# Optimization experiments

Measured on AMD Instinct MI355X. Metric: run time of the kernel, lower is better.

Reference implementation:

```python
import jax, jax.numpy as jnp
import numpy as np

B, T, D, H = 2, 2048, 768, 12
d = D // H
FRAG, K_SEL, G = 16, 6, 4
TOP_U, PROTO = 12, 32
ALPHA, GAMMA = 0.2, 0.2
W_MEAN, W_MAX, W_TOPK, W_STD = 1.0, 0.6, 0.4, 0.2
TOPK_FRAC = 0.2
TAU = 8.0
NEG = -1e9


def _norm(x, eps=1e-6):
    return x / jnp.maximum(jnp.linalg.norm(x, axis=-1, keepdims=True), eps)


def setup_inputs():
    key = jax.random.key(0)
    ks = jax.random.split(key, 5)
    s = 0.02
    return {
        'x': jax.random.normal(ks[0], (B, T, D), jnp.float32),
        'Wq': jax.random.normal(ks[1], (D, D), jnp.float32) * s,
        'bq': jnp.zeros((D,), jnp.float32),
        'Wk': jax.random.normal(ks[2], (D, D), jnp.float32) * s,
        'bk': jnp.zeros((D,), jnp.float32),
        'Wv': jax.random.normal(ks[3], (D, D), jnp.float32) * s,
        'bv': jnp.zeros((D,), jnp.float32),
        'Wo': jax.random.normal(ks[4], (D, D), jnp.float32) * s,
        'bo': jnp.zeros((D,), jnp.float32),
    }


def _forward(x, Wq, bq, Wk, bk, Wv, bv, Wo, bo):
    scaling = d ** -0.5

    def shape(t):  # [B,T,D] -> [B*H,T,d]  (BartAttention._shape layout: (b,h))
        return t.reshape(B, T, H, d).transpose(0, 2, 1, 3).reshape(B * H, T, d)

    q = shape((x @ Wq.T + bq) * scaling)
    k = shape(x @ Wk.T + bk)
    v = shape(x @ Wv.T + bv)

    # ---- windowed local candidate indices (build_indices_encoder) ----
    half = FRAG // 2
    t_ar = jnp.arange(T)
    starts = jnp.clip(t_ar - half, 0, T - FRAG)
    idx = starts[:, None] + jnp.arange(FRAG)[None, :]            # [T,F]
    prior = jnp.exp(-jnp.abs(idx - t_ar[:, None]).astype(jnp.float32) / TAU)

    keys_win = k[:, idx]                                          # [BH,T,F,d]
    scores_win = jnp.einsum('btd,btfd->btf', q, keys_win)
    blended = scores_win + ALPHA * prior[None]

    # ---- greedy diversity-penalized top-k (WindowSelector.select_greedy) ----
    kvn = _norm(keys_win)
    f_ar = jnp.arange(FRAG)
    tmp = blended
    sels = []
    for r in range(K_SEL):
        j = jnp.argmax(tmp, -1)                                   # [BH,T]
        sels.append(j)
        if r < K_SEL - 1:
            sel_vec = jnp.take_along_axis(kvn, j[:, :, None, None], axis=2)[:, :, 0]
            cos = jnp.maximum(jnp.sum(kvn * sel_vec[:, :, None, :], -1), 0.0)
            tmp = tmp - GAMMA * cos
        tmp = jnp.where(f_ar[None, None, :] == j[..., None], NEG, tmp)
    sel_local = jnp.stack(sels, -1)                               # [BH,T,k]
    sel_abs = jnp.take_along_axis(
        jnp.broadcast_to(idx[None], (B * H, T, FRAG)), sel_local, axis=-1)

    # ---- per-head global tokens (GlobalChooser.choose_packed) ----
    # faithful to torch: key_states.view(H, bsz, Tk, d).mean(dim=1)
    Kmean = k.reshape(H, B, T, d).mean(1)
    Kbar = _norm(Kmean)
    q_summary = _norm(q.reshape(H, B, T, d).mean(1))
    idxp = jnp.round(jnp.linspace(0.0, T - 1, PROTO)).astype(jnp.int32)
    Qp = q_summary[:, idxp]                                       # [H,P,d]
    S = jax.nn.relu(jnp.einsum('hkd,hpd->hkp', Kbar, Qp))         # [H,T,P]
    kq = max(1, int(round(PROTO * TOPK_FRAC)))
    u = (W_MEAN * S.mean(-1) + W_MAX * S.max(-1)
         + W_TOPK * jax.lax.top_k(S, kq)[0].mean(-1)
         + W_STD * jnp.std(S, axis=-1, ddof=1))
    U = min(TOP_U, T)
    u_vals, top_idx = jax.lax.top_k(u, U)                         # [H,U]
    S_sub = jnp.take_along_axis(S, top_idx[:, :, None], axis=1)   # [H,U,P]
    hr = jnp.arange(H)
    m = jnp.zeros((H, PROTO), S.dtype)
    blocked = jnp.zeros((H, U), bool)
    chosen = []
    for r in range(G):  # greedy facility-location
        gains = jnp.maximum(S_sub - m[:, None, :], 0.0).sum(-1)
        gains = jnp.where(blocked, NEG, gains)
        j = jnp.argmax(gains, 1)
        chosen.append(j)
        blocked = blocked.at[hr, j].set(True)
        m = jnp.maximum(m, S_sub[hr, j])
    chosen_abs = jnp.take_along_axis(top_idx, jnp.stack(chosen, 1), axis=1)  # [H,G]

    # ---- sparse attention over local + global candidates ----
    glob = jnp.broadcast_to(chosen_abs[None], (B, H, G)).reshape(B * H, G)
    cand = jnp.concatenate(
        [sel_abs, jnp.broadcast_to(glob[:, None, :], (B * H, T, G))], -1)  # [BH,T,k+g]
    Ksel = jax.vmap(lambda kk, ii: kk[ii])(k, cand)               # [BH,T,k+g,d]
    Vsel = jax.vmap(lambda vv, ii: vv[ii])(v, cand)
    attn = jax.nn.softmax(jnp.einsum('btd,btcd->btc', q, Ksel), axis=-1)
    out = jnp.einsum('btc,btcd->btd', attn, Vsel)
    out = out.reshape(B, H, T, d).transpose(0, 2, 1, 3).reshape(B, T, D)
    return out @ Wo.T + bo


def reference(x, Wq, bq, Wk, bk, Wv, bv, Wo, bo):
    return _forward(x, Wq, bq, Wk, bk, Wv, bv, Wo, bo)
```

## Files before the change

kernel.cpp:

```cpp
#include <hip/hip_runtime.h>
#include <math.h>

#define TSEQ 2048
#define DM   768
#define NH   12
#define HD   64
#define NBH  24
#define WN   589824

typedef __attribute__((ext_vector_type(8))) short short8;
typedef __attribute__((ext_vector_type(8))) _Float16 half8;
typedef __attribute__((ext_vector_type(4))) float f32x4;

#define MFMA_F16(a, b, c)  __builtin_amdgcn_mfma_f32_16x16x32_f16(a, b, c, 0, 0, 0)

__constant__ int c_idxp[32] = {0,66,132,198,264,330,396,462,528,594,660,726,
  792,858,924,990,1057,1123,1189,1255,1321,1387,1453,1519,1585,1651,1717,1783,
  1849,1915,1981,2047};

template <int CTRL>
__device__ __forceinline__ float dppf(float x) {
  return __int_as_float(__builtin_amdgcn_mov_dpp(__float_as_int(x), CTRL, 0xF, 0xF, true));
}
template <int CTRL>
__device__ __forceinline__ int dppi(int x) {
  return __builtin_amdgcn_mov_dpp(x, CTRL, 0xF, 0xF, true);
}
__device__ __forceinline__ float wsum(float v) {
  v += dppf<0x121>(v);
  v += dppf<0x122>(v);
  v += dppf<0x124>(v);
  v += dppf<0x128>(v);
  v += __shfl_xor(v, 16, 64);
  v += __shfl_xor(v, 32, 64);
  return v;
}
__device__ __forceinline__ float rowsum16(float v) {
  v += dppf<0x121>(v); v += dppf<0x122>(v);
  v += dppf<0x124>(v); v += dppf<0x128>(v);
  return v;
}
__device__ __forceinline__ float rowmax16(float v) {
  v = fmaxf(v, dppf<0x121>(v)); v = fmaxf(v, dppf<0x122>(v));
  v = fmaxf(v, dppf<0x124>(v)); v = fmaxf(v, dppf<0x128>(v));
  return v;
}
__device__ __forceinline__ int rowmin16i(int v) {
  v = min(v, dppi<0x121>(v)); v = min(v, dppi<0x122>(v));
  v = min(v, dppi<0x124>(v)); v = min(v, dppi<0x128>(v));
  return v;
}

__device__ __forceinline__ void split16(const float4& v0, const float4& v1,
                                        ushort* ph, ushort* pl) {
  float xs[8] = {v0.x, v0.y, v0.z, v0.w, v1.x, v1.y, v1.z, v1.w};
  half8 h, l;
#pragma unroll
  for (int j = 0; j < 8; ++j) {
    _Float16 hb = (_Float16)xs[j];
    h[j] = hb;
    float d = xs[j] - (float)hb;
    l[j] = (_Float16)d;
  }
  *(half8*)ph = h;
  *(half8*)pl = l;
}

__device__ __forceinline__ int lds_idx(int row, int chunk ) {
  int line = row >> 1;
  int c8 = ((row & 1) << 2) | chunk;
  return line * 64 + ((c8 ^ (line & 7)) << 3);
}
__device__ __forceinline__ int qoff(int p, int c8) {
  return p * 64 + (((c8 ^ (p & 7)) & 7) << 3);
}

__global__ __launch_bounds__(256) void convert_kernel(
    const float* __restrict__ x,
    const float* __restrict__ W0, const float* __restrict__ W1,
    const float* __restrict__ W2, const float* __restrict__ W3,
    ushort* __restrict__ Xh, ushort* __restrict__ Xl,
    ushort* __restrict__ wsp) {
  int bid = blockIdx.x;
  if (bid < 1536) {
    size_t base = ((size_t)bid * 256 + threadIdx.x) * 8;
    float4 v0 = *(const float4*)(x + base);
    float4 v1 = *(const float4*)(x + base + 4);
    split16(v0, v1, Xh + base, Xl + base);
  } else {
    int r = bid - 1536;
    int mi = r / 288, sub = r - mi * 288;
    size_t base = ((size_t)sub * 256 + threadIdx.x) * 8;
    const float* s = (mi == 0) ? W0 : (mi == 1) ? W1 : (mi == 2) ? W2 : W3;
    ushort* h = wsp + (size_t)mi * 2 * WN;
    float4 v0 = *(const float4*)(s + base);
    float4 v1 = *(const float4*)(s + base + 4);
    split16(v0, v1, h + base, h + WN + base);
  }
}

template <int MODE, int NPROD>
__device__ __forceinline__ void gemm_mfma_body(
    const ushort* __restrict__ Agh, const ushort* __restrict__ Agl,
    const ushort* __restrict__ Bgh, const ushort* __restrict__ Bgl,
    const float* __restrict__ bias, float* __restrict__ dst, float scale,
    int mblk, int nblk, ushort* lds) {
  const int tid = threadIdx.x;
  const int lane = tid & 63;
  const int w = tid >> 6;
  const int wr = w >> 1, wc = w & 1;
  const int lrow = lane & 15, kq = lane >> 4;
  constexpr int ABUF = 4096;
  constexpr int BBUF = 2048;
  ushort* Ahs = lds;
  ushort* Als = Ahs + ABUF;
  ushort* Bhs = lds + 2 * ABUF;
  ushort* Bls = Bhs + BBUF;

  const int arow = tid >> 2;
  const int achk = tid & 3;
  const int aoff0 = lds_idx(arow, achk);
  const int aoff1 = lds_idx(arow + 64, achk);
  const int boff = lds_idx(arow, achk);

  const size_t a0 = (size_t)(mblk + arow) * DM + achk * 8;
  const size_t a1 = (size_t)(mblk + 64 + arow) * DM + achk * 8;
  const size_t b0 = (size_t)(nblk + arow) * DM + achk * 8;

  f32x4 acc[4][2];
#pragma unroll
  for (int i = 0; i < 4; ++i)
#pragma unroll
    for (int j = 0; j < 2; ++j) {
      f32x4 z = {0.f, 0.f, 0.f, 0.f};
      acc[i][j] = z;
    }

  short8 pah0 = *(const short8*)(Agh + a0), pah1 = *(const short8*)(Agh + a1);
  short8 pal0 = *(const short8*)(Agl + a0), pal1 = *(const short8*)(Agl + a1);
  short8 pbh = *(const short8*)(Bgh + b0);
  short8 pbl = *(const short8*)(Bgl + b0);

  for (int k0 = 0; k0 < DM; k0 += 32) {
    __syncthreads();
    *(short8*)&Ahs[aoff0] = pah0; *(short8*)&Ahs[aoff1] = pah1;
    *(short8*)&Als[aoff0] = pal0; *(short8*)&Als[aoff1] = pal1;
    *(short8*)&Bhs[boff] = pbh;
    *(short8*)&Bls[boff] = pbl;
    __syncthreads();
    if (k0 + 32 < DM) {
      pah0 = *(const short8*)(Agh + a0 + k0 + 32);
      pah1 = *(const short8*)(Agh + a1 + k0 + 32);
      pal0 = *(const short8*)(Agl + a0 + k0 + 32);
      pal1 = *(const short8*)(Agl + a1 + k0 + 32);
      pbh = *(const short8*)(Bgh + b0 + k0 + 32);
      pbl = *(const short8*)(Bgl + b0 + k0 + 32);
    }
    half8 afh[4], afl[4];
#pragma unroll
    for (int fi = 0; fi < 4; ++fi) {
      int o = lds_idx(wr * 64 + fi * 16 + lrow, kq);
      afh[fi] = *(const half8*)&Ahs[o];
      afl[fi] = *(const half8*)&Als[o];
    }
#pragma unroll
    for (int fj = 0; fj < 2; ++fj) {
      int o = lds_idx(wc * 32 + fj * 16 + lrow, kq);
      half8 bfh = *(const half8*)&Bhs[o];
      half8 bfl = *(const half8*)&Bls[o];
#pragma unroll
      for (int fi = 0; fi < 4; ++fi) {
        acc[fi][fj] = MFMA_F16(afh[fi], bfh, acc[fi][fj]);
        acc[fi][fj] = MFMA_F16(afl[fi], bfh, acc[fi][fj]);
        acc[fi][fj] = MFMA_F16(afh[fi], bfl, acc[fi][fj]);
        if (NPROD == 4) {
          acc[fi][fj] = MFMA_F16(afl[fi], bfl, acc[fi][fj]);
        }
      }
    }
  }

#pragma unroll
  for (int fj = 0; fj < 2; ++fj) {
    int col = nblk + wc * 32 + fj * 16 + lrow;
    float bv = bias[col];
#pragma unroll
    for (int fi = 0; fi < 4; ++fi) {
#pragma unroll
      for (int reg = 0; reg < 4; ++reg) {
        int row = mblk + wr * 64 + fi * 16 + kq * 4 + reg;
        float o = (acc[fi][fj][reg] + bv) * scale;
        if (MODE == 0) {
          dst[(size_t)row * DM + col] = o;
        } else {
          int b_ = row >> 11, t = row & (TSEQ - 1);
          int h = col >> 6, dd = col & 63;
          dst[(((size_t)(b_ * NH + h)) * TSEQ + t) * HD + dd] = o;
        }
      }
    }
  }
}

__global__ __launch_bounds__(256) void qkv_kernel(
    const ushort* __restrict__ Xh, const ushort* __restrict__ Xl,
    const ushort* __restrict__ wsp,
    const float* __restrict__ bq, float* __restrict__ qd,
    const float* __restrict__ bk, float* __restrict__ kd,
    const float* __restrict__ bv, float* __restrict__ vd) {
  __shared__ ushort lds[2 * 4096 + 2 * 2048];
  int lid = blockIdx.x + 12 * blockIdx.y + 384 * blockIdx.z;
  int swz = (lid & 7) * 144 + (lid >> 3);
  int z = swz / 384;
  int rem = swz - z * 384;
  int wy = rem / 12, wx = rem - wy * 12;
  const ushort* Bb = wsp + (size_t)z * 2 * WN;
  if (z == 2) {
    gemm_mfma_body<1, 3>(Xh, Xl, Bb, Bb + WN,
                         bv, vd, 1.0f, wy * 128, wx * 64, lds);
  } else {
    gemm_mfma_body<1, 4>(Xh, Xl, Bb, Bb + WN,
                         z ? bk : bq, z ? kd : qd, z ? 1.0f : 0.125f,
                         wy * 128, wx * 64, lds);
  }
}

__global__ __launch_bounds__(256) void oproj_kernel(
    const ushort* __restrict__ Ph, const ushort* __restrict__ Pl,
    const ushort* __restrict__ wsp,
    const float* __restrict__ bias, float* __restrict__ dst) {
  __shared__ ushort lds[2 * 4096 + 2 * 2048];
  int lid = blockIdx.x + 12 * blockIdx.y;
  int swz = (lid & 7) * 48 + (lid >> 3);
  int wy = swz / 12, wx = swz - wy * 12;
  const ushort* Bb = wsp + (size_t)3 * 2 * WN;
  gemm_mfma_body<0, 3>(Ph, Pl, Bb, Bb + WN,
                       bias, dst, 1.0f, wy * 128, wx * 64, lds);
}

__global__ __launch_bounds__(256) void select_kernel(
    const float* __restrict__ q, const float* __restrict__ k,
    int* __restrict__ sel, float* __restrict__ S, float* __restrict__ u,
    int* __restrict__ glob, int* __restrict__ cnt) {
  __shared__ ushort Qh[2048], Ql[2048];
  int wv = threadIdx.x >> 6, lane = threadIdx.x & 63;

  if (blockIdx.x < 12288) {
    int wid = blockIdx.x * 4 + wv;
    int f = lane & 15, kq = lane >> 4;
    int bh = wid >> 11, t = wid & (TSEQ - 1);
    int start = t - 8;
    if (start < 0) start = 0;
    if (start > TSEQ - 16) start = TSEQ - 16;

    const float* kp = k + ((size_t)bh * TSEQ + start + f) * HD + kq * 8;
    const float* qp = q + ((size_t)bh * TSEQ + t) * HD + kq * 8;
    float kv[16], qv[16];
    *(float4*)&kv[0]  = *(const float4*)(kp + 0);
    *(float4*)&kv[4]  = *(const float4*)(kp + 4);
    *(float4*)&kv[8]  = *(const float4*)(kp + 32);
    *(float4*)&kv[12] = *(const float4*)(kp + 36);
    *(float4*)&qv[0]  = *(const float4*)(qp + 0);
    *(float4*)&qv[4]  = *(const float4*)(qp + 4);
    *(float4*)&qv[8]  = *(const float4*)(qp + 32);
    *(float4*)&qv[12] = *(const float4*)(qp + 36);

    float sp = 0.f, np = 0.f;
#pragma unroll
    for (int i = 0; i < 16; ++i) { sp = fmaf(qv[i], kv[i], sp); np = fmaf(kv[i], kv[i], np); }
    sp += __shfl_xor(sp, 16, 64); sp += __shfl_xor(sp, 32, 64);
    np += __shfl_xor(np, 16, 64); np += __shfl_xor(np, 32, 64);
    float nrm = fmaxf(sqrtf(np), 1e-6f);
    float kn[16];
#pragma unroll
    for (int i = 0; i < 16; ++i) kn[i] = kv[i] / nrm;

    half8 h0, l0, h1, l1;
#pragma unroll
    for (int j = 0; j < 8; ++j) {
      _Float16 hb = (_Float16)kn[j];
      h0[j] = hb;
      l0[j] = (_Float16)(kn[j] - (float)hb);
      _Float16 hb1 = (_Float16)kn[8 + j];
      h1[j] = hb1;
      l1[j] = (_Float16)(kn[8 + j] - (float)hb1);
    }
    f32x4 g = {0.f, 0.f, 0.f, 0.f};
    g = MFMA_F16(h0, h0, g); g = MFMA_F16(h1, h1, g);
    g = MFMA_F16(l0, h0, g); g = MFMA_F16(l1, h1, g);
    g = MFMA_F16(h0, l0, g); g = MFMA_F16(h1, l1, g);
    g = MFMA_F16(l0, l0, g); g = MFMA_F16(l1, l1, g);

    int dist = start + f - t; if (dist < 0) dist = -dist;
    float tmp = sp + 0.2f * expf(-(float)dist * 0.125f);

    int* selp = sel + ((size_t)bh * TSEQ + t) * 6;
#pragma unroll
    for (int r = 0; r < 6; ++r) {
      float best = tmp; int bj = f;
      {
        float ov = dppf<0x121>(best); int oi = dppi<0x121>(bj);
        if (ov > best || (ov == best && oi < bj)) { best = ov; bj = oi; }
        ov = dppf<0x122>(best); oi = dppi<0x122>(bj);
        if (ov > best || (ov == best && oi < bj)) { best = ov; bj = oi; }
        ov = dppf<0x124>(best); oi = dppi<0x124>(bj);
        if (ov > best || (ov == best && oi < bj)) { best = ov; bj = oi; }
        ov = dppf<0x128>(best); oi = dppi<0x128>(bj);
        if (ov > best || (ov == best && oi < bj)) { best = ov; bj = oi; }
      }
      if (lane == 0) selp[r] = start + bj;
      if (r < 5) {
        float s01 = (bj & 1) ? g[1] : g[0];
        float s23 = (bj & 1) ? g[3] : g[2];
        float gsel = (bj & 2) ? s23 : s01;
        float grow = __shfl(gsel, ((bj >> 2) << 4) | f, 64);
        tmp -= 0.2f * fmaxf(grow, 0.f);
      }
      if (f == bj) tmp = -1e9f;
    }
    return;
  }

  int bid2 = blockIdx.x - 12288;
  int a = bid2 >> 5;
  int tb = bid2 & 31;

  {
    int p = wv * 8 + (lane >> 3);
    int c8 = lane & 7;
    int t = c_idxp[p];
    const float* q0 = q + ((size_t)(2 * a) * TSEQ + t) * HD + c8 * 8;
    const float* q1 = q + ((size_t)(2 * a + 1) * TSEQ + t) * HD + c8 * 8;
    float4 x0 = *(const float4*)q0, x1 = *(const float4*)(q0 + 4);
    float4 y0 = *(const float4*)q1, y1 = *(const float4*)(q1 + 4);
    float vv[8] = {0.5f * (x0.x + y0.x), 0.5f * (x0.y + y0.y),
                   0.5f * (x0.z + y0.z), 0.5f * (x0.w + y0.w),
                   0.5f * (x1.x + y1.x), 0.5f * (x1.y + y1.y),
                   0.5f * (x1.z + y1.z), 0.5f * (x1.w + y1.w)};
    float ssq = 0.f;
#pragma unroll
    for (int j = 0; j < 8; ++j) ssq = fmaf(vv[j], vv[j], ssq);
    ssq += __shfl_xor(ssq, 1, 64);
    ssq += __shfl_xor(ssq, 2, 64);
    ssq += __shfl_xor(ssq, 4, 64);
    float nrm = fmaxf(sqrtf(ssq), 1e-6f);
    half8 qh, ql_;
#pragma unroll
    for (int j = 0; j < 8; ++j) {
      float xx = vv[j] / nrm;
      _Float16 hb = (_Float16)xx;
      qh[j] = hb;
      ql_[j] = (_Float16)(xx - (float)hb);
    }
    *(half8*)&Qh[qoff(p, c8)] = qh;
    *(half8*)&Ql[qoff(p, c8)] = ql_;
  }
  __syncthreads();

  int f = lane & 15, kq = lane >> 4;
  int tbase = tb * 64 + wv * 16;
  int tl = tbase + f;

  const float* k0p = k + ((size_t)(2 * a) * TSEQ + tl) * HD + kq * 8;
  const float* k1p = k + ((size_t)(2 * a + 1) * TSEQ + tl) * HD + kq * 8;
  float km[16];
  {
    float4 x0 = *(const float4*)(k0p + 0),  y0 = *(const float4*)(k1p + 0);
    float4 x1 = *(const float4*)(k0p + 4),  y1 = *(const float4*)(k1p + 4);
    float4 x2 = *(const float4*)(k0p + 32), y2 = *(const float4*)(k1p + 32);
    float4 x3 = *(const float4*)(k0p + 36), y3 = *(const float4*)(k1p + 36);
    km[0] = 0.5f*(x0.x+y0.x); km[1] = 0.5f*(x0.y+y0.y);
    km[2] = 0.5f*(x0.z+y0.z); km[3] = 0.5f*(x0.w+y0.w);
    km[4] = 0.5f*(x1.x+y1.x); km[5] = 0.5f*(x1.y+y1.y);
    km[6] = 0.5f*(x1.z+y1.z); km[7] = 0.5f*(x1.w+y1.w);
    km[8] = 0.5f*(x2.x+y2.x); km[9] = 0.5f*(x2.y+y2.y);
    km[10] = 0.5f*(x2.z+y2.z); km[11] = 0.5f*(x2.w+y2.w);
    km[12] = 0.5f*(x3.x+y3.x); km[13] = 0.5f*(x3.y+y3.y);
    km[14] = 0.5f*(x3.z+y3.z); km[15] = 0.5f*(x3.w+y3.w);
  }
  float np = 0.f;
#pragma unroll
  for (int i = 0; i < 16; ++i) np = fmaf(km[i], km[i], np);
  np += __shfl_xor(np, 16, 64); np += __shfl_xor(np, 32, 64);
  float nrm = fmaxf(sqrtf(np), 1e-6f);

  half8 ah[2], al[2];
#pragma unroll
  for (int s = 0; s < 2; ++s)
#pragma unroll
    for (int j = 0; j < 8; ++j) {
      float x = km[s * 8 + j] / nrm;
      _Float16 hb = (_Float16)x;
      ah[s][j] = hb;
      al[s][j] = (_Float16)(x - (float)hb);
    }

  f32x4 acc0 = {0.f, 0.f, 0.f, 0.f}, acc1 = {0.f, 0.f, 0.f, 0.f};
#pragma unroll
  for (int s = 0; s < 2; ++s) {
    half8 b0h = *(const half8*)&Qh[qoff(f, s * 4 + kq)];
    half8 b0l = *(const half8*)&Ql[qoff(f, s * 4 + kq)];
    half8 b1h = *(const half8*)&Qh[qoff(16 + f, s * 4 + kq)];
    half8 b1l = *(const half8*)&Ql[qoff(16 + f, s * 4 + kq)];
    acc0 = MFMA_F16(ah[s], b0h, acc0);
    acc0 = MFMA_F16(al[s], b0h, acc0);
    acc0 = MFMA_F16(ah[s], b0l, acc0);
    acc0 = MFMA_F16(al[s], b0l, acc0);
    acc1 = MFMA_F16(ah[s], b1h, acc1);
    acc1 = MFMA_F16(al[s], b1h, acc1);
    acc1 = MFMA_F16(ah[s], b1l, acc1);
    acc1 = MFMA_F16(al[s], b1l, acc1);
  }

#pragma unroll
  for (int reg = 0; reg < 4; ++reg) {
    float s0 = fmaxf(acc0[reg], 0.f);
    float s1 = fmaxf(acc1[reg], 0.f);
    int t = tbase + kq * 4 + reg;
    size_t srow = ((size_t)a * TSEQ + t) * 32;
    S[srow + f] = s0;
    S[srow + 16 + f] = s1;
    float mean = rowsum16(s0 + s1) / 32.0f;
    float mx = rowmax16(fmaxf(s0, s1));
    float cur0 = s0, cur1 = s1;
    float topsum = 0.f;
#pragma unroll
    for (int r = 0; r < 6; ++r) {
      float mm = rowmax16(fmaxf(cur0, cur1));
      topsum += mm;
      int i0 = rowmin16i((cur0 == mm) ? f : 999);
      int i1 = rowmin16i((cur1 == mm) ? f : 999);
      bool take0 = (i0 < 999);
      if (take0 && f == i0) cur0 = -1e30f;
      if (!take0 && f == i1) cur1 = -1e30f;
    }
    float d0 = s0 - mean, d1 = s1 - mean;
    float sd = sqrtf(rowsum16(d0 * d0 + d1 * d1) / 31.0f);
    float uval = ((1.0f * mean + 0.6f * mx) + 0.4f * (topsum / 6.0f)) + 0.2f * sd;
    if (f == 0) u[(size_t)a * TSEQ + t] = uval;
  }

  __threadfence();
  __syncthreads();
  if (threadIdx.x < 64) {
    int old = 0;
    if (lane == 0) old = atomicAdd(&cnt[a], 1);
    old = __shfl(old, 0, 64);
    if (old == 31) {
      __threadfence();
      float uv[32];
#pragma unroll
      for (int c = 0; c < 32; ++c) uv[c] = u[(size_t)a * TSEQ + c * 64 + lane];
      unsigned removed = 0;
      int tidx = 0;
#pragma unroll
      for (int r = 0; r < 12; ++r) {
        float best = -1e30f; int bidx = 1 << 30;
#pragma unroll
        for (int c = 0; c < 32; ++c) {
          if (!((removed >> c) & 1u)) {
            float vv = uv[c]; int gi = c * 64 + lane;
            if (vv > best || (vv == best && gi < bidx)) { best = vv; bidx = gi; }
          }
        }
#pragma unroll
        for (int mS = 1; mS < 64; mS <<= 1) {
          float ov = __shfl_xor(best, mS, 64);
          int oi = __shfl_xor(bidx, mS, 64);
          if (ov > best || (ov == best && oi < bidx)) { best = ov; bidx = oi; }
        }
        if (lane == (bidx & 63)) removed |= 1u << (bidx >> 6);
        if (lane == r) tidx = bidx;
      }
      float srow[12];
#pragma unroll
      for (int r = 0; r < 12; ++r) {
        int tr = __shfl(tidx, r, 64);
        srow[r] = (lane < 32) ? S[((size_t)a * TSEQ + tr) * 32 + lane] : 0.f;
      }
      float m = 0.f;
      unsigned blocked = 0;
#pragma unroll
      for (int g = 0; g < 4; ++g) {
        float gains[12];
#pragma unroll
        for (int r = 0; r < 12; ++r) {
          float gr = (lane < 32) ? fmaxf(srow[r] - m, 0.f) : 0.f;
          gains[r] = wsum(gr);
        }
        float best = -1e30f; int bj = 0;
#pragma unroll
        for (int r = 0; r < 12; ++r) {
          float vv = ((blocked >> r) & 1u) ? -1e9f : gains[r];
          if (vv > best) { best = vv; bj = r; }
        }
        blocked |= 1u << bj;
#pragma unroll
        for (int r = 0; r < 12; ++r) m = (r == bj) ? fmaxf(m, srow[r]) : m;
        int gidx = __shfl(tidx, bj, 64);
        if (lane == 0) glob[a * 4 + g] = gidx;
      }
    }
  }
}

__global__ __launch_bounds__(256) void attend_kernel(
    const float* __restrict__ q, const float* __restrict__ k,
    const float* __restrict__ v, const int* __restrict__ sel,
    const int* __restrict__ glob, ushort* __restrict__ Ph,
    ushort* __restrict__ Pl) {
  int wid = blockIdx.x * 4 + (threadIdx.x >> 6);
  int lane = threadIdx.x & 63;
  int bh = wid >> 11, t = wid & (TSEQ - 1);
  int h = bh % NH, b = bh / NH;
  float qv = q[((size_t)bh * TSEQ + t) * HD + lane];
  int cand[10];
  const int* selp = sel + ((size_t)bh * TSEQ + t) * 6;
#pragma unroll
  for (int c = 0; c < 6; ++c) cand[c] = selp[c];
#pragma unroll
  for (int c = 0; c < 4; ++c) cand[6 + c] = glob[h * 4 + c];
  float sc[10];
#pragma unroll
  for (int c = 0; c < 10; ++c) {
    float kv = k[((size_t)bh * TSEQ + cand[c]) * HD + lane];
    sc[c] = wsum(qv * kv);
  }
  float mx = sc[0];
#pragma unroll
  for (int c = 1; c < 10; ++c) mx = fmaxf(mx, sc[c]);
  float e[10], den = 0.f;
#pragma unroll
  for (int c = 0; c < 10; ++c) { e[c] = expf(sc[c] - mx); den += e[c]; }
  float o = 0.f;
#pragma unroll
  for (int c = 0; c < 10; ++c) {
    float w = e[c] / den;
    o += w * v[((size_t)bh * TSEQ + cand[c]) * HD + lane];
  }
  size_t idx = ((size_t)b * TSEQ + t) * DM + h * HD + lane;
  _Float16 hb = (_Float16)o;
  float d = o - (float)hb;
  Ph[idx] = __builtin_bit_cast(ushort, hb);
  _Float16 lb = (_Float16)d;
  Pl[idx] = __builtin_bit_cast(ushort, lb);
}

extern "C" void kernel_launch(void* const* d_in, const int* in_sizes, int n_in,
                              void* d_out, int out_size, void* d_ws, size_t ws_size,
                              hipStream_t stream) {
  const float* x  = (const float*)d_in[0];
  const float* Wq = (const float*)d_in[1];
  const float* bq = (const float*)d_in[2];
  const float* Wk = (const float*)d_in[3];
  const float* bk = (const float*)d_in[4];
  const float* Wv = (const float*)d_in[5];
  const float* bv = (const float*)d_in[6];
  const float* Wo = (const float*)d_in[7];
  const float* bo = (const float*)d_in[8];
  float* out = (float*)d_out;

  float* ws = (float*)d_ws;
  const size_t QKV = (size_t)NBH * TSEQ * HD;
  float* qb = ws;
  float* kb = qb + QKV;
  float* vb = kb + QKV;
  float* slotA = vb + QKV;
  float* QpSlot = slotA + QKV;
  float* S  = QpSlot + (size_t)NH * 32 * HD;
  float* u  = S + (size_t)NH * TSEQ * 32;
  int* sel  = (int*)(u + (size_t)NH * TSEQ);
  int* glob = sel + (size_t)NBH * TSEQ * 6;
  int* cnt  = glob + 48;
  ushort* wsp = (ushort*)(glob + 64);

  ushort* Xh = (ushort*)slotA;
  ushort* Xl = Xh + QKV;
  ushort* Ph = Xh;
  ushort* Pl = Xl;

  hipMemsetAsync(cnt, 0, 12 * sizeof(int), stream);
  convert_kernel<<<2688, 256, 0, stream>>>(x, Wq, Wk, Wv, Wo, Xh, Xl, wsp);
  qkv_kernel<<<dim3(12, 32, 3), 256, 0, stream>>>(
      Xh, Xl, wsp, bq, qb, bk, kb, bv, vb);
  select_kernel<<<12672, 256, 0, stream>>>(qb, kb, sel, S, u, glob, cnt);
  attend_kernel<<<12288, 256, 0, stream>>>(qb, kb, vb, sel, glob, Ph, Pl);
  oproj_kernel<<<dim3(12, 32), 256, 0, stream>>>(Ph, Pl, wsp, bo, out);
}
```

Baseline: 251.2 us.

## Merge Q and K projections into one GEMM tile and split select kernel

Q and K projection tiles now share one pass over the A tile: each block loads the split-precision X tile once and accumulates both the Q and K products, cutting the qkv grid from 3 to 2 z-slices. The combined select kernel is split into a window-selection kernel and a separate prototype/global-selection kernel launched back-to-back. This reduces redundant A-tile loads and LDS staging but doubles accumulator registers per thread, which may lower occupancy. The split adds one kernel launch and serializes the two selection phases.

```diff
diff --git a/kernel.cpp b/kernel.cpp
--- a/kernel.cpp
+++ b/kernel.cpp
@@ -202,26 +202,139 @@
   }
 }
 
+__device__ __forceinline__ void qk_merged_body(
+    const ushort* __restrict__ Agh, const ushort* __restrict__ Agl,
+    const ushort* __restrict__ Bqh_g, const ushort* __restrict__ Bql_g,
+    const ushort* __restrict__ Bkh_g, const ushort* __restrict__ Bkl_g,
+    const float* __restrict__ bq, float* __restrict__ qd,
+    const float* __restrict__ bk, float* __restrict__ kd,
+    int mblk, int nblk, ushort* lds) {
+  const int tid = threadIdx.x;
+  const int lane = tid & 63;
+  const int w = tid >> 6;
+  const int wr = w >> 1, wc = w & 1;
+  const int lrow = lane & 15, kq = lane >> 4;
+  ushort* Ahs = lds;
+  ushort* Als = lds + 4096;
+  ushort* Bqh = lds + 8192;
+  ushort* Bql = lds + 10240;
+  ushort* Bkh = lds + 12288;
+  ushort* Bkl = lds + 14336;
+
+  const int arow = tid >> 2;
+  const int achk = tid & 3;
+  const int aoff0 = lds_idx(arow, achk);
+  const int aoff1 = lds_idx(arow + 64, achk);
+  const int boff = lds_idx(arow, achk);
+
+  const size_t a0 = (size_t)(mblk + arow) * DM + achk * 8;
+  const size_t a1 = (size_t)(mblk + 64 + arow) * DM + achk * 8;
+  const size_t b0 = (size_t)(nblk + arow) * DM + achk * 8;
+
+  f32x4 accq[4][2], acck[4][2];
+#pragma unroll
+  for (int i = 0; i < 4; ++i)
+#pragma unroll
+    for (int j = 0; j < 2; ++j) {
+      f32x4 z = {0.f, 0.f, 0.f, 0.f};
+      accq[i][j] = z;
+      acck[i][j] = z;
+    }
+
+  short8 pah0 = *(const short8*)(Agh + a0), pah1 = *(const short8*)(Agh + a1);
+  short8 pal0 = *(const short8*)(Agl + a0), pal1 = *(const short8*)(Agl + a1);
+  short8 pbqh = *(const short8*)(Bqh_g + b0);
+  short8 pbql = *(const short8*)(Bql_g + b0);
+  short8 pbkh = *(const short8*)(Bkh_g + b0);
+  short8 pbkl = *(const short8*)(Bkl_g + b0);
+
+  for (int k0 = 0; k0 < DM; k0 += 32) {
+    __syncthreads();
+    *(short8*)&Ahs[aoff0] = pah0; *(short8*)&Ahs[aoff1] = pah1;
+    *(short8*)&Als[aoff0] = pal0; *(short8*)&Als[aoff1] = pal1;
+    *(short8*)&Bqh[boff] = pbqh;
+    *(short8*)&Bql[boff] = pbql;
+    *(short8*)&Bkh[boff] = pbkh;
+    *(short8*)&Bkl[boff] = pbkl;
+    __syncthreads();
+    if (k0 + 32 < DM) {
+      pah0 = *(const short8*)(Agh + a0 + k0 + 32);
+      pah1 = *(const short8*)(Agh + a1 + k0 + 32);
+      pal0 = *(const short8*)(Agl + a0 + k0 + 32);
+      pal1 = *(const short8*)(Agl + a1 + k0 + 32);
+      pbqh = *(const short8*)(Bqh_g + b0 + k0 + 32);
+      pbql = *(const short8*)(Bql_g + b0 + k0 + 32);
+      pbkh = *(const short8*)(Bkh_g + b0 + k0 + 32);
+      pbkl = *(const short8*)(Bkl_g + b0 + k0 + 32);
+    }
+    half8 afh[4], afl[4];
+#pragma unroll
+    for (int fi = 0; fi < 4; ++fi) {
+      int o = lds_idx(wr * 64 + fi * 16 + lrow, kq);
+      afh[fi] = *(const half8*)&Ahs[o];
+      afl[fi] = *(const half8*)&Als[o];
+    }
+#pragma unroll
+    for (int fj = 0; fj < 2; ++fj) {
+      int o = lds_idx(wc * 32 + fj * 16 + lrow, kq);
+      half8 bfh = *(const half8*)&Bqh[o];
+      half8 bfl = *(const half8*)&Bql[o];
+      half8 cfh = *(const half8*)&Bkh[o];
+      half8 cfl = *(const half8*)&Bkl[o];
+#pragma unroll
+      for (int fi = 0; fi < 4; ++fi) {
+        accq[fi][fj] = MFMA_F16(afh[fi], bfh, accq[fi][fj]);
+        accq[fi][fj] = MFMA_F16(afl[fi], bfh, accq[fi][fj]);
+        accq[fi][fj] = MFMA_F16(afh[fi], bfl, accq[fi][fj]);
+        accq[fi][fj] = MFMA_F16(afl[fi], bfl, accq[fi][fj]);
+        acck[fi][fj] = MFMA_F16(afh[fi], cfh, acck[fi][fj]);
+        acck[fi][fj] = MFMA_F16(afl[fi], cfh, acck[fi][fj]);
+        acck[fi][fj] = MFMA_F16(afh[fi], cfl, acck[fi][fj]);
+        acck[fi][fj] = MFMA_F16(afl[fi], cfl, acck[fi][fj]);
+      }
+    }
+  }
+
+#pragma unroll
+  for (int fj = 0; fj < 2; ++fj) {
+    int col = nblk + wc * 32 + fj * 16 + lrow;
+    float bqv = bq[col], bkv = bk[col];
+#pragma unroll
+    for (int fi = 0; fi < 4; ++fi) {
+#pragma unroll
+      for (int reg = 0; reg < 4; ++reg) {
+        int row = mblk + wr * 64 + fi * 16 + kq * 4 + reg;
+        int b_ = row >> 11, t = row & (TSEQ - 1);
+        int h = col >> 6, dd = col & 63;
+        size_t idx = (((size_t)(b_ * NH + h)) * TSEQ + t) * HD + dd;
+        qd[idx] = (accq[fi][fj][reg] + bqv) * 0.125f;
+        kd[idx] = (acck[fi][fj][reg] + bkv) * 1.0f;
+      }
+    }
+  }
+}
+
 __global__ __launch_bounds__(256) void qkv_kernel(
     const ushort* __restrict__ Xh, const ushort* __restrict__ Xl,
     const ushort* __restrict__ wsp,
     const float* __restrict__ bq, float* __restrict__ qd,
     const float* __restrict__ bk, float* __restrict__ kd,
     const float* __restrict__ bv, float* __restrict__ vd) {
-  __shared__ ushort lds[2 * 4096 + 2 * 2048];
+  __shared__ ushort lds[16384];
   int lid = blockIdx.x + 12 * blockIdx.y + 384 * blockIdx.z;
-  int swz = (lid & 7) * 144 + (lid >> 3);
+  int swz = (lid & 7) * 96 + (lid >> 3);
   int z = swz / 384;
   int rem = swz - z * 384;
   int wy = rem / 12, wx = rem - wy * 12;
-  const ushort* Bb = wsp + (size_t)z * 2 * WN;
-  if (z == 2) {
+  if (z == 1) {
+    const ushort* Bb = wsp + (size_t)2 * 2 * WN;
     gemm_mfma_body<1, 3>(Xh, Xl, Bb, Bb + WN,
                          bv, vd, 1.0f, wy * 128, wx * 64, lds);
   } else {
-    gemm_mfma_body<1, 4>(Xh, Xl, Bb, Bb + WN,
-                         z ? bk : bq, z ? kd : qd, z ? 1.0f : 0.125f,
-                         wy * 128, wx * 64, lds);
+    const ushort* Bq = wsp;
+    const ushort* Bk = wsp + (size_t)2 * WN;
+    qk_merged_body(Xh, Xl, Bq, Bq + WN, Bk, Bk + WN,
+                   bq, qd, bk, kd, wy * 128, wx * 64, lds);
   }
 }
 
@@ -238,92 +351,92 @@
                        bias, dst, 1.0f, wy * 128, wx * 64, lds);
 }
 
-__global__ __launch_bounds__(256) void select_kernel(
+__global__ __launch_bounds__(256) void window_kernel(
     const float* __restrict__ q, const float* __restrict__ k,
-    int* __restrict__ sel, float* __restrict__ S, float* __restrict__ u,
+    int* __restrict__ sel) {
+  int wid = blockIdx.x * 4 + (threadIdx.x >> 6);
+  int lane = threadIdx.x & 63;
+  int f = lane & 15, kq = lane >> 4;
+  int bh = wid >> 11, t = wid & (TSEQ - 1);
+  int start = t - 8;
+  if (start < 0) start = 0;
+  if (start > TSEQ - 16) start = TSEQ - 16;
+
+  const float* kp = k + ((size_t)bh * TSEQ + start + f) * HD + kq * 8;
+  const float* qp = q + ((size_t)bh * TSEQ + t) * HD + kq * 8;
+  float kv[16], qv[16];
+  *(float4*)&kv[0]  = *(const float4*)(kp + 0);
+  *(float4*)&kv[4]  = *(const float4*)(kp + 4);
+  *(float4*)&kv[8]  = *(const float4*)(kp + 32);
+  *(float4*)&kv[12] = *(const float4*)(kp + 36);
+  *(float4*)&qv[0]  = *(const float4*)(qp + 0);
+  *(float4*)&qv[4]  = *(const float4*)(qp + 4);
+  *(float4*)&qv[8]  = *(const float4*)(qp + 32);
+  *(float4*)&qv[12] = *(const float4*)(qp + 36);
+
+  float sp = 0.f, np = 0.f;
+#pragma unroll
+  for (int i = 0; i < 16; ++i) { sp = fmaf(qv[i], kv[i], sp); np = fmaf(kv[i], kv[i], np); }
+  sp += __shfl_xor(sp, 16, 64); sp += __shfl_xor(sp, 32, 64);
+  np += __shfl_xor(np, 16, 64); np += __shfl_xor(np, 32, 64);
+  float nrm = fmaxf(sqrtf(np), 1e-6f);
+  float kn[16];
+#pragma unroll
+  for (int i = 0; i < 16; ++i) kn[i] = kv[i] / nrm;
+
+  half8 h0, l0, h1, l1;
+#pragma unroll
+  for (int j = 0; j < 8; ++j) {
+    _Float16 hb = (_Float16)kn[j];
+    h0[j] = hb;
+    l0[j] = (_Float16)(kn[j] - (float)hb);
+    _Float16 hb1 = (_Float16)kn[8 + j];
+    h1[j] = hb1;
+    l1[j] = (_Float16)(kn[8 + j] - (float)hb1);
+  }
+  f32x4 g = {0.f, 0.f, 0.f, 0.f};
+  g = MFMA_F16(h0, h0, g); g = MFMA_F16(h1, h1, g);
+  g = MFMA_F16(l0, h0, g); g = MFMA_F16(l1, h1, g);
+  g = MFMA_F16(h0, l0, g); g = MFMA_F16(h1, l1, g);
+  g = MFMA_F16(l0, l0, g); g = MFMA_F16(l1, l1, g);
+
+  int dist = start + f - t; if (dist < 0) dist = -dist;
+  float tmp = sp + 0.2f * expf(-(float)dist * 0.125f);
+
+  int* selp = sel + ((size_t)bh * TSEQ + t) * 6;
+#pragma unroll
+  for (int r = 0; r < 6; ++r) {
+    float best = tmp; int bj = f;
+    {
+      float ov = dppf<0x121>(best); int oi = dppi<0x121>(bj);
+      if (ov > best || (ov == best && oi < bj)) { best = ov; bj = oi; }
+      ov = dppf<0x122>(best); oi = dppi<0x122>(bj);
+      if (ov > best || (ov == best && oi < bj)) { best = ov; bj = oi; }
+      ov = dppf<0x124>(best); oi = dppi<0x124>(bj);
+      if (ov > best || (ov == best && oi < bj)) { best = ov; bj = oi; }
+      ov = dppf<0x128>(best); oi = dppi<0x128>(bj);
+      if (ov > best || (ov == best && oi < bj)) { best = ov; bj = oi; }
+    }
+    if (lane == 0) selp[r] = start + bj;
+    if (r < 5) {
+      float s01 = (bj & 1) ? g[1] : g[0];
+      float s23 = (bj & 1) ? g[3] : g[2];
+      float gsel = (bj & 2) ? s23 : s01;
+      float grow = __shfl(gsel, ((bj >> 2) << 4) | f, 64);
+      tmp -= 0.2f * fmaxf(grow, 0.f);
+    }
+    if (f == bj) tmp = -1e9f;
+  }
+}
+
+__global__ __launch_bounds__(256) void proto_select_kernel(
+    const float* __restrict__ q, const float* __restrict__ k,
+    float* __restrict__ S, float* __restrict__ u,
     int* __restrict__ glob, int* __restrict__ cnt) {
   __shared__ ushort Qh[2048], Ql[2048];
   int wv = threadIdx.x >> 6, lane = threadIdx.x & 63;
-
-  if (blockIdx.x < 12288) {
-    int wid = blockIdx.x * 4 + wv;
-    int f = lane & 15, kq = lane >> 4;
-    int bh = wid >> 11, t = wid & (TSEQ - 1);
-    int start = t - 8;
-    if (start < 0) start = 0;
-    if (start > TSEQ - 16) start = TSEQ - 16;
-
-    const float* kp = k + ((size_t)bh * TSEQ + start + f) * HD + kq * 8;
-    const float* qp = q + ((size_t)bh * TSEQ + t) * HD + kq * 8;
-    float kv[16], qv[16];
-    *(float4*)&kv[0]  = *(const float4*)(kp + 0);
-    *(float4*)&kv[4]  = *(const float4*)(kp + 4);
-    *(float4*)&kv[8]  = *(const float4*)(kp + 32);
-    *(float4*)&kv[12] = *(const float4*)(kp + 36);
-    *(float4*)&qv[0]  = *(const float4*)(qp + 0);
-    *(float4*)&qv[4]  = *(const float4*)(qp + 4);
-    *(float4*)&qv[8]  = *(const float4*)(qp + 32);
-    *(float4*)&qv[12] = *(const float4*)(qp + 36);
-
-    float sp = 0.f, np = 0.f;
-#pragma unroll
-    for (int i = 0; i < 16; ++i) { sp = fmaf(qv[i], kv[i], sp); np = fmaf(kv[i], kv[i], np); }
-    sp += __shfl_xor(sp, 16, 64); sp += __shfl_xor(sp, 32, 64);
-    np += __shfl_xor(np, 16, 64); np += __shfl_xor(np, 32, 64);
-    float nrm = fmaxf(sqrtf(np), 1e-6f);
-    float kn[16];
-#pragma unroll
-    for (int i = 0; i < 16; ++i) kn[i] = kv[i] / nrm;
-
-    half8 h0, l0, h1, l1;
-#pragma unroll
-    for (int j = 0; j < 8; ++j) {
-      _Float16 hb = (_Float16)kn[j];
-      h0[j] = hb;
-      l0[j] = (_Float16)(kn[j] - (float)hb);
-      _Float16 hb1 = (_Float16)kn[8 + j];
-      h1[j] = hb1;
-      l1[j] = (_Float16)(kn[8 + j] - (float)hb1);
-    }
-    f32x4 g = {0.f, 0.f, 0.f, 0.f};
-    g = MFMA_F16(h0, h0, g); g = MFMA_F16(h1, h1, g);
-    g = MFMA_F16(l0, h0, g); g = MFMA_F16(l1, h1, g);
-    g = MFMA_F16(h0, l0, g); g = MFMA_F16(h1, l1, g);
-    g = MFMA_F16(l0, l0, g); g = MFMA_F16(l1, l1, g);
-
-    int dist = start + f - t; if (dist < 0) dist = -dist;
-    float tmp = sp + 0.2f * expf(-(float)dist * 0.125f);
-
-    int* selp = sel + ((size_t)bh * TSEQ + t) * 6;
-#pragma unroll
-    for (int r = 0; r < 6; ++r) {
-      float best = tmp; int bj = f;
-      {
-        float ov = dppf<0x121>(best); int oi = dppi<0x121>(bj);
-        if (ov > best || (ov == best && oi < bj)) { best = ov; bj = oi; }
-        ov = dppf<0x122>(best); oi = dppi<0x122>(bj);
-        if (ov > best || (ov == best && oi < bj)) { best = ov; bj = oi; }
-        ov = dppf<0x124>(best); oi = dppi<0x124>(bj);
-        if (ov > best || (ov == best && oi < bj)) { best = ov; bj = oi; }
-        ov = dppf<0x128>(best); oi = dppi<0x128>(bj);
-        if (ov > best || (ov == best && oi < bj)) { best = ov; bj = oi; }
-      }
-      if (lane == 0) selp[r] = start + bj;
-      if (r < 5) {
-        float s01 = (bj & 1) ? g[1] : g[0];
-        float s23 = (bj & 1) ? g[3] : g[2];
-        float gsel = (bj & 2) ? s23 : s01;
-        float grow = __shfl(gsel, ((bj >> 2) << 4) | f, 64);
-        tmp -= 0.2f * fmaxf(grow, 0.f);
-      }
-      if (f == bj) tmp = -1e9f;
-    }
-    return;
-  }
-
-  int bid2 = blockIdx.x - 12288;
-  int a = bid2 >> 5;
-  int tb = bid2 & 31;
+  int a = blockIdx.x >> 5;
+  int tb = blockIdx.x & 31;
 
   {
     int p = wv * 8 + (lane >> 3);
@@ -581,9 +694,10 @@
 
   hipMemsetAsync(cnt, 0, 12 * sizeof(int), stream);
   convert_kernel<<<2688, 256, 0, stream>>>(x, Wq, Wk, Wv, Wo, Xh, Xl, wsp);
-  qkv_kernel<<<dim3(12, 32, 3), 256, 0, stream>>>(
+  qkv_kernel<<<dim3(12, 32, 2), 256, 0, stream>>>(
       Xh, Xl, wsp, bq, qb, bk, kb, bv, vb);
-  select_kernel<<<12672, 256, 0, stream>>>(qb, kb, sel, S, u, glob, cnt);
+  window_kernel<<<12288, 256, 0, stream>>>(qb, kb, sel);
+  proto_select_kernel<<<384, 256, 0, stream>>>(qb, kb, S, u, glob, cnt);
   attend_kernel<<<12288, 256, 0, stream>>>(qb, kb, vb, sel, glob, Ph, Pl);
   oproj_kernel<<<dim3(12, 32), 256, 0, stream>>>(Ph, Pl, wsp, bo, out);
 }
```

Measured after the change: 256.3 us. +2.0%, slower.
